# Performance work log

Measured on AMD Instinct MI355X. Metric: run time of the kernel, lower is better.

## Reference

```python
import jax, jax.numpy as jnp
import numpy as np
import math

DIM = 512
HEADS = 8
B = 16
P = 2048
REL_MAX = 64
REL_SIZE = 2 * REL_MAX + 1
RANK = 4
ALPHA = 16.0
QBITS = 4


def simq(w, bits=QBITS):
    # symmetric linear fake-quantization (matches simulate_quantization)
    qmin = -2 ** (bits - 1)
    qmax = 2 ** (bits - 1) - 1
    m = jnp.max(jnp.abs(w))
    scale = m / qmax
    q = jnp.clip(jnp.round(w / (scale + 1e-8)), qmin, qmax) * scale
    return jnp.where(m == 0, w, q)


def lora_lin(x, W, b, A, LB):
    # F.linear with quantized weight/bias + LoRA path
    out = x @ simq(W).T + simq(b)
    return out + (x @ A.T @ LB.T) * (ALPHA / RANK)


def setup_inputs() -> dict:
    key = jax.random.key(0)
    ks = jax.random.split(key, 20)
    d2 = DIM * 2
    inp = {
        "curr_pos": 2048,
        "z_curr_ri": jax.random.normal(ks[0], (B, DIM, 2), jnp.float32),
        "z_past_ri": jax.random.normal(ks[1], (P, B, DIM, 2), jnp.float32),
        "rel_bias_ri": jax.random.normal(ks[2], (REL_SIZE, DIM, 2), jnp.float32) * 0.02,
    }
    names = ["q", "k", "v", "o"]
    for i, n in enumerate(names):
        kw, ka, kb = jax.random.split(ks[3 + i], 3)
        inp["W" + n] = jax.random.normal(kw, (d2, d2), jnp.float32) / math.sqrt(d2)
        inp["b" + n] = jnp.zeros((d2,), jnp.float32)
        inp["A" + n] = jax.random.normal(ka, (RANK, d2), jnp.float32) / math.sqrt(d2)
        inp["LB" + n] = jax.random.normal(kb, (d2, RANK), jnp.float32) * 0.01
    return inp


def reference(curr_pos, z_curr_ri, z_past_ri, rel_bias_ri,
              Wq, bq, Aq, LBq, Wk, bk, Ak, LBk,
              Wv, bv, Av, LBv, Wo, bo, Ao, LBo):
    Bsz = z_curr_ri.shape[0]
    past_len = z_past_ri.shape[0]
    dim = z_curr_ri.shape[1]
    hd = dim // HEADS

    # projections on real-view of complex inputs ([.., dim, 2] -> [.., 2*dim])
    q = lora_lin(z_curr_ri.reshape(Bsz, dim * 2), Wq, bq, Aq, LBq)
    k = lora_lin(z_past_ri.reshape(past_len, Bsz, dim * 2), Wk, bk, Ak, LBk)
    v = lora_lin(z_past_ri.reshape(past_len, Bsz, dim * 2), Wv, bv, Av, LBv)

    q = q.reshape(Bsz, HEADS, hd, 2)            # [B,H,hd,2]
    k = k.reshape(past_len, Bsz, HEADS, hd, 2)  # [P,B,H,hd,2]
    v = v.reshape(past_len, Bsz, HEADS, hd, 2)
    qr, qi = q[..., 0], q[..., 1]
    kr, ki = k[..., 0], k[..., 1]
    vr, vi = v[..., 0], v[..., 1]

    # Re(q * conj(k)) summed over head_dim -> [B,H,P]
    dot = jnp.einsum('bhd,pbhd->bhp', qr, kr) + jnp.einsum('bhd,pbhd->bhp', qi, ki)

    # relative positional bias lookup (clamped index)
    rel_d = jnp.arange(curr_pos - past_len, curr_pos)
    idx = jnp.clip(rel_d + REL_MAX, 0, rel_bias_ri.shape[0] - 1)
    rb = rel_bias_ri[idx].reshape(past_len, HEADS, hd, 2)  # [P,H,hd,2]
    rel = jnp.einsum('bhd,phd->bhp', qr, rb[..., 0]) + jnp.einsum('bhd,phd->bhp', qi, rb[..., 1])

    w = jax.nn.softmax((dot + rel) / math.sqrt(hd), axis=-1)  # [B,H,P]

    # real softmax weights applied to complex values
    out_r = jnp.einsum('bhp,pbhd->bhd', w, vr)
    out_i = jnp.einsum('bhp,pbhd->bhd', w, vi)
    out_ri = jnp.stack([out_r, out_i], axis=-1).reshape(Bsz, dim * 2)

    o = lora_lin(out_ri, Wo, bo, Ao, LBo)
    return o.reshape(Bsz, dim, 2)  # real view of complex output [B,dim]
```

## Files before the change

kernel.cpp:

```cpp
#include <hip/hip_runtime.h>
#include <math.h>

typedef _Float16 f16;
typedef _Float16 f16x8 __attribute__((ext_vector_type(8)));
typedef _Float16 f16x4 __attribute__((ext_vector_type(4)));
typedef float f32x4 __attribute__((ext_vector_type(4)));

#define NP 2048
#define M_ROWS 32768

#define OFF_ABSMAX 0u
#define OFF_TQ     256u
#define OFF_TO     512u
#define OFF_QBIAS  1024u
#define OFF_XQH    32768u
#define OFF_XQL    65536u
#define OFF_XOH    98304u
#define OFF_XOL    131072u
#define OFF_QBUF   163840u
#define OFF_ATT    229376u
#define OFF_PM     294912u
#define OFF_PL     299008u
#define OFF_PO     303104u
#define OFF_WH     1048576u
#define OFF_TK     9437184u
#define OFF_TV     9961472u
#define OFF_KV     10485760u

__device__ __forceinline__ float qint_of(float w, float scale) {
    return fminf(7.f, fmaxf(-8.f, rintf(w / (scale + 1e-8f))));
}

__device__ __forceinline__ void gload16(const void* g, void* l) {
  __builtin_amdgcn_global_load_lds((const __attribute__((address_space(1))) void*)g,
                                   (__attribute__((address_space(3))) void*)l, 16, 0, 0);
}

__global__ void __launch_bounds__(256) absmax_kernel(
    const float* __restrict__ W0, const float* __restrict__ W1,
    const float* __restrict__ W2, const float* __restrict__ W3,
    unsigned* __restrict__ absmax) {
  int mat = blockIdx.x >> 6;
  int blk = blockIdx.x & 63;
  const float* W = mat == 0 ? W0 : mat == 1 ? W1 : mat == 2 ? W2 : W3;
  int tid = blk * 256 + threadIdx.x;
  const float4* W4 = (const float4*)W;
  float m = 0.f;
  #pragma unroll
  for (int i = 0; i < 16; ++i) {
    float4 v = W4[tid + i * 16384];
    m = fmaxf(m, fmaxf(fmaxf(fabsf(v.x), fabsf(v.y)), fmaxf(fabsf(v.z), fabsf(v.w))));
  }
  #pragma unroll
  for (int k = 32; k >= 1; k >>= 1) m = fmaxf(m, __shfl_xor(m, k));
  __shared__ float sm[4];
  if ((threadIdx.x & 63) == 0) sm[threadIdx.x >> 6] = m;
  __syncthreads();
  if (threadIdx.x == 0) {
    m = fmaxf(fmaxf(sm[0], sm[1]), fmaxf(sm[2], sm[3]));
    atomicMax(&absmax[mat], __float_as_uint(m));
  }
}

__global__ void __launch_bounds__(256) bias_quant_kernel(
    const float* __restrict__ b0, const float* __restrict__ b1,
    const float* __restrict__ b2, const float* __restrict__ b3,
    float* __restrict__ qbias) {
  int mat = blockIdx.x;
  const float* bb = mat == 0 ? b0 : mat == 1 ? b1 : mat == 2 ? b2 : b3;
  int t = threadIdx.x;
  float4 v = ((const float4*)bb)[t];
  float m = fmaxf(fmaxf(fabsf(v.x), fabsf(v.y)), fmaxf(fabsf(v.z), fabsf(v.w)));
  #pragma unroll
  for (int k = 32; k >= 1; k >>= 1) m = fmaxf(m, __shfl_xor(m, k));
  __shared__ float sm[4];
  if ((t & 63) == 0) sm[t >> 6] = m;
  __syncthreads();
  float M = fmaxf(fmaxf(sm[0], sm[1]), fmaxf(sm[2], sm[3]));
  float scale = M * (1.0f / 7.0f);
  float4 q;
  q.x = (M == 0.f) ? v.x : qint_of(v.x, scale) * scale;
  q.y = (M == 0.f) ? v.y : qint_of(v.y, scale) * scale;
  q.z = (M == 0.f) ? v.z : qint_of(v.z, scale) * scale;
  q.w = (M == 0.f) ? v.w : qint_of(v.w, scale) * scale;
  ((float4*)(qbias + mat * 1024))[t] = q;
}

__global__ void __launch_bounds__(256) quantW_kernel(
    const float* __restrict__ W0, const float* __restrict__ W1,
    const float* __restrict__ W2, const float* __restrict__ W3,
    const unsigned* __restrict__ absmax, f16* __restrict__ Wh) {
  int gid = blockIdx.x * 256 + threadIdx.x;
  int mat = gid >> 18;
  int idx = gid & 262143;
  const float* W = mat == 0 ? W0 : mat == 1 ? W1 : mat == 2 ? W2 : W3;
  float scale = __uint_as_float(absmax[mat]) * (1.0f / 7.0f);
  float4 v = ((const float4*)W)[idx];
  f16x4 r;
  r[0] = (f16)qint_of(v.x, scale);
  r[1] = (f16)qint_of(v.y, scale);
  r[2] = (f16)qint_of(v.z, scale);
  r[3] = (f16)qint_of(v.w, scale);
  *(f16x4*)(Wh + (size_t)mat * 1048576 + (size_t)idx * 4) = r;
}

__global__ void __launch_bounds__(256) cvt_hilo_kernel(
    const float* __restrict__ x, f16* __restrict__ hi, f16* __restrict__ lo) {
  int i = blockIdx.x * 256 + threadIdx.x;
  float4 v = ((const float4*)x)[i];
  f16 h0 = (f16)v.x, h1 = (f16)v.y, h2 = (f16)v.z, h3 = (f16)v.w;
  f16x4 hv = {h0, h1, h2, h3};
  f16x4 lv = {(f16)(v.x - (float)h0), (f16)(v.y - (float)h1),
              (f16)(v.z - (float)h2), (f16)(v.w - (float)h3)};
  *(f16x4*)(hi + (size_t)i * 4) = hv;
  *(f16x4*)(lo + (size_t)i * 4) = lv;
}

__global__ void __launch_bounds__(256) lora_t_small_kernel(
    const float* __restrict__ x, const float* __restrict__ A, float* __restrict__ t) {
  int tt = threadIdx.x;
  int b = tt >> 4;
  int r = (tt >> 2) & 3;
  int s = tt & 3;
  const float4* xv = (const float4*)(x + b * 1024 + s * 256);
  const float4* av = (const float4*)(A + r * 1024 + s * 256);
  float acc = 0.f;
  #pragma unroll 4
  for (int i = 0; i < 64; ++i) {
    float4 a = xv[i], c = av[i];
    acc += a.x * c.x + a.y * c.y + a.z * c.z + a.w * c.w;
  }
  acc += __shfl_xor(acc, 1);
  acc += __shfl_xor(acc, 2);
  if (s == 0) t[b * 4 + r] = acc;
}

__global__ void __launch_bounds__(256) lora_t_big_kernel(
    const float* __restrict__ zp, const float* __restrict__ Ak,
    const float* __restrict__ Av, float* __restrict__ tk, float* __restrict__ tv,
    f16* __restrict__ zph, f16* __restrict__ zpl) {
  __shared__ float sA[8 * 1024];
  for (int i = 0; i < 8; ++i) {
    int f4 = threadIdx.x + i * 256;
    float4 v = (f4 < 1024) ? ((const float4*)Ak)[f4] : ((const float4*)Av)[f4 - 1024];
    ((float4*)sA)[f4] = v;
  }
  __syncthreads();
  int lane = threadIdx.x & 63, wave = threadIdx.x >> 6;
  for (int it = 0; it < 4; ++it) {
    int m = blockIdx.x * 16 + wave * 4 + it;
    const float4* xr = (const float4*)(zp + (size_t)m * 1024);
    float acc[8] = {0.f, 0.f, 0.f, 0.f, 0.f, 0.f, 0.f, 0.f};
    for (int c = lane; c < 256; c += 64) {
      float4 xv = xr[c];
      if (zph) {
        f16 h0 = (f16)xv.x, h1 = (f16)xv.y, h2 = (f16)xv.z, h3 = (f16)xv.w;
        f16x4 hv = {h0, h1, h2, h3};
        f16x4 lv = {(f16)(xv.x - (float)h0), (f16)(xv.y - (float)h1),
                    (f16)(xv.z - (float)h2), (f16)(xv.w - (float)h3)};
        *(f16x4*)(zph + (size_t)m * 1024 + c * 4) = hv;
        *(f16x4*)(zpl + (size_t)m * 1024 + c * 4) = lv;
      }
      #pragma unroll
      for (int r = 0; r < 8; ++r) {
        float4 a = ((const float4*)sA)[r * 256 + c];
        acc[r] += xv.x * a.x + xv.y * a.y + xv.z * a.z + xv.w * a.w;
      }
    }
    #pragma unroll
    for (int k = 32; k >= 1; k >>= 1) {
      #pragma unroll
      for (int r = 0; r < 8; ++r) acc[r] += __shfl_xor(acc[r], k);
    }
    if (lane == 0) {
      tk[m * 4 + 0] = acc[0]; tk[m * 4 + 1] = acc[1];
      tk[m * 4 + 2] = acc[2]; tk[m * 4 + 3] = acc[3];
      tv[m * 4 + 0] = acc[4]; tv[m * 4 + 1] = acc[5];
      tv[m * 4 + 2] = acc[6]; tv[m * 4 + 3] = acc[7];
    }
  }
}

__global__ void __launch_bounds__(256) gemv_mfma_kernel(
    const f16* __restrict__ xhi, const f16* __restrict__ xlo,
    const f16* __restrict__ Wm, const unsigned* __restrict__ absmax, int mat,
    const float* __restrict__ qb, const float* __restrict__ t,
    const float* __restrict__ LB, float* __restrict__ out) {
  int wave = threadIdx.x >> 6, lane = threadIdx.x & 63;
  int nf = blockIdx.x * 4 + wave;
  int n0 = nf * 16;
  int row = lane & 15, kq = lane >> 4;
  f32x4 acc = {0.f, 0.f, 0.f, 0.f};
  const f16* xh = xhi + row * 1024 + kq * 8;
  const f16* xl = xlo + row * 1024 + kq * 8;
  const f16* wp = Wm + (size_t)(n0 + row) * 1024 + kq * 8;
  #pragma unroll 4
  for (int k0 = 0; k0 < 1024; k0 += 32) {
    f16x8 ah = *(const f16x8*)(xh + k0);
    f16x8 al = *(const f16x8*)(xl + k0);
    f16x8 bb = *(const f16x8*)(wp + k0);
    acc = __builtin_amdgcn_mfma_f32_16x16x32_f16(ah, bb, acc, 0, 0, 0);
    acc = __builtin_amdgcn_mfma_f32_16x16x32_f16(al, bb, acc, 0, 0, 0);
  }
  float scale = __uint_as_float(absmax[mat]) * (1.0f / 7.0f);
  int col = n0 + row;
  float bias = qb[col];
  float4 lb = *(const float4*)(LB + col * 4);
  #pragma unroll
  for (int j = 0; j < 4; ++j) {
    int m = kq * 4 + j;
    float4 tvv = *(const float4*)(t + m * 4);
    out[m * 1024 + col] =
        scale * acc[j] + bias + 4.0f * (tvv.x * lb.x + tvv.y * lb.y + tvv.z * lb.z + tvv.w * lb.w);
  }
}

__global__ void __launch_bounds__(256, 2) kv_gemm_kernel(
    const float* __restrict__ zp, const f16* __restrict__ Wh,
    const unsigned* __restrict__ absmax, const float* __restrict__ qbias,
    const float* __restrict__ tk, const float* __restrict__ tv,
    const float* __restrict__ LBk, const float* __restrict__ LBv,
    f16* __restrict__ kout, f16* __restrict__ vout) {
  __shared__ __align__(16) f16 sAh[128][40];
  __shared__ __align__(16) f16 sAl[128][40];
  __shared__ __align__(16) f16 sB[128][40];
  __shared__ float sT[128][4];

  int nb = blockIdx.x;
  int m0 = blockIdx.y * 128;
  bool is_v = nb >= 8;
  int n0 = (nb & 7) * 128;
  int mat = is_v ? 2 : 1;
  const f16* Wm = Wh + (size_t)mat * 1048576;
  const float* ttv = is_v ? tv : tk;
  const float* LBm = is_v ? LBv : LBk;
  const float* qb = qbias + mat * 1024;
  f16* outp = is_v ? vout : kout;

  int tid = threadIdx.x;
  int lane = tid & 63, wave = tid >> 6;
  int wm = (wave >> 1) * 64, wn = (wave & 1) * 64;
  int row = lane & 15, kq = lane >> 4;

  f32x4 acc[4][4];
  #pragma unroll
  for (int i = 0; i < 4; ++i)
    #pragma unroll
    for (int j = 0; j < 4; ++j) acc[i][j] = (f32x4){0.f, 0.f, 0.f, 0.f};

  int sr = tid >> 1, seg = tid & 1;
  const float* asrc = zp + (size_t)(m0 + sr) * 1024 + seg * 16;
  const f16* bsrc = Wm + (size_t)(n0 + sr) * 1024 + seg * 16;

  for (int k0 = 0; k0 < 1024; k0 += 32) {
    __syncthreads();
    float xs[16];
    const float4* a4 = (const float4*)(asrc + k0);
    *(float4*)&xs[0] = a4[0];
    *(float4*)&xs[4] = a4[1];
    *(float4*)&xs[8] = a4[2];
    *(float4*)&xs[12] = a4[3];
    f16 hs[16], ls[16];
    #pragma unroll
    for (int i = 0; i < 16; ++i) {
      f16 h = (f16)xs[i];
      hs[i] = h;
      ls[i] = (f16)(xs[i] - (float)h);
    }
    *(f16x8*)&sAh[sr][seg * 16] = *(f16x8*)&hs[0];
    *(f16x8*)&sAh[sr][seg * 16 + 8] = *(f16x8*)&hs[8];
    *(f16x8*)&sAl[sr][seg * 16] = *(f16x8*)&ls[0];
    *(f16x8*)&sAl[sr][seg * 16 + 8] = *(f16x8*)&ls[8];
    const f16x8* b8 = (const f16x8*)(bsrc + k0);
    *(f16x8*)&sB[sr][seg * 16] = b8[0];
    *(f16x8*)&sB[sr][seg * 16 + 8] = b8[1];
    __syncthreads();
    f16x8 ah[4], al[4], bf[4];
    #pragma unroll
    for (int mi = 0; mi < 4; ++mi) {
      ah[mi] = *(const f16x8*)&sAh[wm + mi * 16 + row][kq * 8];
      al[mi] = *(const f16x8*)&sAl[wm + mi * 16 + row][kq * 8];
    }
    #pragma unroll
    for (int ni = 0; ni < 4; ++ni) bf[ni] = *(const f16x8*)&sB[wn + ni * 16 + row][kq * 8];
    #pragma unroll
    for (int mi = 0; mi < 4; ++mi)
      #pragma unroll
      for (int ni = 0; ni < 4; ++ni)
        acc[mi][ni] = __builtin_amdgcn_mfma_f32_16x16x32_f16(ah[mi], bf[ni], acc[mi][ni], 0, 0, 0);
    #pragma unroll
    for (int mi = 0; mi < 4; ++mi)
      #pragma unroll
      for (int ni = 0; ni < 4; ++ni)
        acc[mi][ni] = __builtin_amdgcn_mfma_f32_16x16x32_f16(al[mi], bf[ni], acc[mi][ni], 0, 0, 0);
  }
  ((float2*)sT)[tid] = ((const float2*)(ttv + (size_t)m0 * 4))[tid];
  __syncthreads();
  float scale = __uint_as_float(absmax[mat]) * (1.0f / 7.0f);
  #pragma unroll
  for (int ni = 0; ni < 4; ++ni) {
    int ncol = n0 + wn + ni * 16 + row;
    int h = ncol >> 7, d = ncol & 127;
    float4 lb = *(const float4*)(LBm + ncol * 4);
    float bias = qb[ncol];
    #pragma unroll
    for (int mi = 0; mi < 4; ++mi) {
      #pragma unroll
      for (int j = 0; j < 4; ++j) {
        int mloc = wm + mi * 16 + kq * 4 + j;
        int m = m0 + mloc;
        int p = m >> 4, b = m & 15;
        float4 t4 = *(const float4*)&sT[mloc][0];
        float val = scale * acc[mi][ni][j] + bias +
                    4.0f * (t4.x * lb.x + t4.y * lb.y + t4.z * lb.z + t4.w * lb.w);
        outp[(((size_t)(b * 8 + h)) * 2048 + p) * 128 + d] = (f16)val;
      }
    }
  }
}

__global__ void __launch_bounds__(256, 3) kv_gemm_fast_kernel(
    const f16* __restrict__ zph, const f16* __restrict__ zpl,
    const f16* __restrict__ Wh, const unsigned* __restrict__ absmax,
    const float* __restrict__ qbias, const float* __restrict__ tk,
    const float* __restrict__ tv, const float* __restrict__ LBk,
    const float* __restrict__ LBv, f16* __restrict__ kout, f16* __restrict__ vout) {
  __shared__ __align__(16) f16 sbuf[24576];
  __shared__ float sT[128][4];

  int linear = blockIdx.x + (blockIdx.y << 4);
  int xcd = linear & 7;
  int slot = linear >> 3;
  int nb = slot & 15;
  int g = ((slot >> 4) << 3) + xcd;
  int m0 = g << 7;

  bool is_v = nb >= 8;
  int n0 = (nb & 7) * 128;
  int mat = is_v ? 2 : 1;
  int h = nb & 7;
  const f16* Wm = Wh + (size_t)mat * 1048576;
  const float* ttv = is_v ? tv : tk;
  const float* LBm = is_v ? LBv : LBk;
  const float* qb = qbias + mat * 1024;
  f16* outp = is_v ? vout : kout;

  int tid = threadIdx.x;
  int lane = tid & 63, wave = tid >> 6;
  int wm = (wave >> 1) * 64, wn = (wave & 1) * 64;
  int row = lane & 15, kq = lane >> 4;

  const f16* src0 = zph + (size_t)m0 * 1024;
  const f16* src1 = zpl + (size_t)m0 * 1024;
  const f16* src2 = Wm + (size_t)n0 * 1024;

  int goff[2], lbase[2];
  #pragma unroll
  for (int r = 0; r < 2; ++r) {
    int L = r * 256 + tid;
    int rw = L >> 2, cc = L & 3;
    int cs = cc ^ (rw & 3) ^ ((rw >> 2) & 3);
    goff[r] = rw * 1024 + cs * 8;
    lbase[r] = r * 2048 + wave * 512;
  }

  f32x4 acc[4][4];
  #pragma unroll
  for (int i = 0; i < 4; ++i)
    #pragma unroll
    for (int j = 0; j < 4; ++j) acc[i][j] = (f32x4){0.f, 0.f, 0.f, 0.f};

  int radA[4], radB[4];
  #pragma unroll
  for (int mi = 0; mi < 4; ++mi) {
    int R = wm + mi * 16 + row;
    radA[mi] = R * 32 + ((kq ^ (R & 3) ^ ((R >> 2) & 3)) << 3);
    int Rb = wn + mi * 16 + row;
    radB[mi] = Rb * 32 + ((kq ^ (Rb & 3) ^ ((Rb >> 2) & 3)) << 3);
  }

  #pragma unroll
  for (int r = 0; r < 2; ++r) {
    gload16(src0 + goff[r], sbuf + lbase[r]);
    gload16(src1 + goff[r], sbuf + 4096 + lbase[r]);
    gload16(src2 + goff[r], sbuf + 8192 + lbase[r]);
  }
  __syncthreads();

  int cur = 0;
  for (int t = 0; t < 32; ++t) {
    if (t < 31) {
      int nxt = (cur ^ 1) * 12288;
      int gk = (t + 1) * 32;
      #pragma unroll
      for (int r = 0; r < 2; ++r) {
        gload16(src0 + goff[r] + gk, sbuf + nxt + lbase[r]);
        gload16(src1 + goff[r] + gk, sbuf + nxt + 4096 + lbase[r]);
        gload16(src2 + goff[r] + gk, sbuf + nxt + 8192 + lbase[r]);
      }
    }
    const f16* bAh = sbuf + cur * 12288;
    const f16* bAl = bAh + 4096;
    const f16* bB = bAh + 8192;
    f16x8 ah[4], al[4], bf[4];
    #pragma unroll
    for (int mi = 0; mi < 4; ++mi) {
      ah[mi] = *(const f16x8*)&bAh[radA[mi]];
      al[mi] = *(const f16x8*)&bAl[radA[mi]];
    }
    #pragma unroll
    for (int ni = 0; ni < 4; ++ni) bf[ni] = *(const f16x8*)&bB[radB[ni]];
    #pragma unroll
    for (int mi = 0; mi < 4; ++mi)
      #pragma unroll
      for (int ni = 0; ni < 4; ++ni)
        acc[mi][ni] = __builtin_amdgcn_mfma_f32_16x16x32_f16(ah[mi], bf[ni], acc[mi][ni], 0, 0, 0);
    #pragma unroll
    for (int mi = 0; mi < 4; ++mi)
      #pragma unroll
      for (int ni = 0; ni < 4; ++ni)
        acc[mi][ni] = __builtin_amdgcn_mfma_f32_16x16x32_f16(al[mi], bf[ni], acc[mi][ni], 0, 0, 0);
    __syncthreads();
    cur ^= 1;
  }

  ((float2*)sT)[tid] = ((const float2*)(ttv + (size_t)m0 * 4))[tid];
  __syncthreads();
  float scale = __uint_as_float(absmax[mat]) * (1.0f / 7.0f);
  float biasv[4];
  float4 lbv[4];
  #pragma unroll
  for (int ni = 0; ni < 4; ++ni) {
    int ncol = n0 + wn + ni * 16 + row;
    biasv[ni] = qb[ncol];
    lbv[ni] = *(const float4*)(LBm + ncol * 4);
  }
  float* tbuf = (float*)sbuf;
  int lh = lane >> 5, l5 = lane & 31;
  #pragma unroll
  for (int halfsel = 0; halfsel < 2; ++halfsel) {
    __syncthreads();
    if ((wave >> 1) == halfsel) {
      #pragma unroll
      for (int ni = 0; ni < 4; ++ni) {
        #pragma unroll
        for (int mi = 0; mi < 4; ++mi) {
          #pragma unroll
          for (int j = 0; j < 4; ++j) {
            int ml = mi * 16 + kq * 4 + j;
            float4 t4 = *(const float4*)&sT[wm + ml][0];
            tbuf[ml * 132 + wn + ni * 16 + row] =
                scale * acc[mi][ni][j] + biasv[ni] +
                4.0f * (t4.x * lbv[ni].x + t4.y * lbv[ni].y + t4.z * lbv[ni].z +
                        t4.w * lbv[ni].w);
          }
        }
      }
    }
    __syncthreads();
    #pragma unroll
    for (int it = 0; it < 8; ++it) {
      int ml = it * 8 + wave * 2 + lh;
      int m = m0 + halfsel * 64 + ml;
      int p = m >> 4, b = m & 15;
      float4 v = *(const float4*)&tbuf[ml * 132 + l5 * 4];
      f16x4 hv = {(f16)v.x, (f16)v.y, (f16)v.z, (f16)v.w};
      *(f16x4*)(outp + (((size_t)(b * 8 + h)) * 2048 + p) * 128 + l5 * 4) = hv;
    }
  }
}

__device__ __forceinline__ float4 ld4h(const f16* p) {
  f16x4 v = *reinterpret_cast<const f16x4*>(p);
  return make_float4((float)v[0], (float)v[1], (float)v[2], (float)v[3]);
}

__global__ void __launch_bounds__(256) attn_part_kernel(
    const float* __restrict__ qbuf, const f16* __restrict__ kbuf,
    const f16* __restrict__ vbuf, const float* __restrict__ rel_bias,
    const int* __restrict__ curr_pos_p, float* __restrict__ m_part,
    float* __restrict__ l_part, float* __restrict__ o_part) {
  __shared__ float sS[256];
  __shared__ float red[8];
  __shared__ float sOv[8][132];
  int bh = blockIdx.x;
  int c = blockIdx.y;
  int b = bh >> 3, h = bh & 7;
  int p0 = c * 256;
  int tid = threadIdx.x, lane = tid & 63, wave = tid >> 6;
  int j4 = lane & 31, ph = lane >> 5;
  float4 qv = *(const float4*)(qbuf + b * 1024 + h * 128 + j4 * 4);
  int off = *curr_pos_p - NP + 64;
  const f16* kb = kbuf + ((size_t)bh * 2048 + p0) * 128;
  for (int i = 0; i < 32; ++i) {
    int pl = i * 8 + wave * 2 + ph;
    float4 kv = ld4h(kb + (size_t)pl * 128 + j4 * 4);
    int idx = min(max(p0 + pl + off, 0), 128);
    float4 rb = *(const float4*)(rel_bias + idx * 1024 + h * 128 + j4 * 4);
    float a = qv.x * (kv.x + rb.x) + qv.y * (kv.y + rb.y) +
              qv.z * (kv.z + rb.z) + qv.w * (kv.w + rb.w);
    a += __shfl_xor(a, 16);
    a += __shfl_xor(a, 8);
    a += __shfl_xor(a, 4);
    a += __shfl_xor(a, 2);
    a += __shfl_xor(a, 1);
    if (j4 == 0) sS[pl] = a * 0.125f;
  }
  __syncthreads();
  float v = sS[tid];
  float mx = v;
  #pragma unroll
  for (int k = 32; k >= 1; k >>= 1) mx = fmaxf(mx, __shfl_xor(mx, k));
  if (lane == 0) red[wave] = mx;
  __syncthreads();
  mx = fmaxf(fmaxf(red[0], red[1]), fmaxf(red[2], red[3]));
  float e = expf(v - mx);
  sS[tid] = e;
  float sum = e;
  #pragma unroll
  for (int k = 32; k >= 1; k >>= 1) sum += __shfl_xor(sum, k);
  if (lane == 0) red[4 + wave] = sum;
  __syncthreads();
  float l = red[4] + red[5] + red[6] + red[7];
  int d4 = tid & 31, pg = tid >> 5;
  const f16* vb = vbuf + ((size_t)bh * 2048 + p0 + pg * 32) * 128;
  float4 a4 = make_float4(0.f, 0.f, 0.f, 0.f);
  #pragma unroll 4
  for (int i = 0; i < 32; ++i) {
    float s = sS[pg * 32 + i];
    float4 vv = ld4h(vb + (size_t)i * 128 + d4 * 4);
    a4.x += s * vv.x;
    a4.y += s * vv.y;
    a4.z += s * vv.z;
    a4.w += s * vv.w;
  }
  *(float4*)&sOv[pg][d4 * 4] = a4;
  __syncthreads();
  if (tid < 128) {
    float o = 0.f;
    #pragma unroll
    for (int gI = 0; gI < 8; ++gI) o += sOv[gI][tid];
    int pc = bh * 8 + c;
    o_part[pc * 128 + tid] = o;
    if (tid == 0) {
      m_part[pc] = mx;
      l_part[pc] = l;
    }
  }
}

__global__ void __launch_bounds__(128) attn_combine_kernel(
    const float* __restrict__ m_part, const float* __restrict__ l_part,
    const float* __restrict__ o_part, float* __restrict__ attout) {
  int bh = blockIdx.x;
  int d = threadIdx.x;
  float M = -1e30f;
  #pragma unroll
  for (int c = 0; c < 8; ++c) M = fmaxf(M, m_part[bh * 8 + c]);
  float L = 0.f, o = 0.f;
  #pragma unroll
  for (int c = 0; c < 8; ++c) {
    float w = expf(m_part[bh * 8 + c] - M);
    L += w * l_part[bh * 8 + c];
    o += w * o_part[(bh * 8 + c) * 128 + d];
  }
  int b = bh >> 3, h = bh & 7;
  attout[b * 1024 + h * 128 + d] = o / L;
}

extern "C" void kernel_launch(void* const* d_in, const int* in_sizes, int n_in,
                              void* d_out, int out_size, void* d_ws, size_t ws_size,
                              hipStream_t stream) {
  const int* curr_pos = (const int*)d_in[0];
  const float* z_curr = (const float*)d_in[1];
  const float* z_past = (const float*)d_in[2];
  const float* rel_bias = (const float*)d_in[3];
  const float* Wq = (const float*)d_in[4];
  const float* bq = (const float*)d_in[5];
  const float* Aq = (const float*)d_in[6];
  const float* LBq = (const float*)d_in[7];
  const float* Wk = (const float*)d_in[8];
  const float* bk = (const float*)d_in[9];
  const float* Ak = (const float*)d_in[10];
  const float* LBk = (const float*)d_in[11];
  const float* Wv = (const float*)d_in[12];
  const float* bv = (const float*)d_in[13];
  const float* Av = (const float*)d_in[14];
  const float* LBv = (const float*)d_in[15];
  const float* Wo = (const float*)d_in[16];
  const float* bo = (const float*)d_in[17];
  const float* Ao = (const float*)d_in[18];
  const float* LBo = (const float*)d_in[19];

  char* ws = (char*)d_ws;
  unsigned* absmax = (unsigned*)(ws + OFF_ABSMAX);
  float* t_q = (float*)(ws + OFF_TQ);
  float* t_o = (float*)(ws + OFF_TO);
  float* qbias = (float*)(ws + OFF_QBIAS);
  f16* xqh = (f16*)(ws + OFF_XQH);
  f16* xql = (f16*)(ws + OFF_XQL);
  f16* xoh = (f16*)(ws + OFF_XOH);
  f16* xol = (f16*)(ws + OFF_XOL);
  float* qbuf = (float*)(ws + OFF_QBUF);
  float* attout = (float*)(ws + OFF_ATT);
  float* pm = (float*)(ws + OFF_PM);
  float* pl = (float*)(ws + OFF_PL);
  float* po = (float*)(ws + OFF_PO);
  f16* Wh = (f16*)(ws + OFF_WH);
  float* t_k = (float*)(ws + OFF_TK);
  float* t_v = (float*)(ws + OFF_TV);
  char* kvbase = ws + OFF_KV;

  f16* kb = (f16*)kvbase;
  f16* vb = (f16*)(kvbase + 67108864ull);
  f16* zph = (f16*)(kvbase + 2ull * 67108864ull);
  f16* zpl = (f16*)(kvbase + 3ull * 67108864ull);
  bool fast = ws_size >= (size_t)OFF_KV + 4ull * 67108864ull;

  hipMemsetAsync(absmax, 0, 16, stream);
  absmax_kernel<<<256, 256, 0, stream>>>(Wq, Wk, Wv, Wo, absmax);
  bias_quant_kernel<<<4, 256, 0, stream>>>(bq, bk, bv, bo, qbias);
  quantW_kernel<<<4096, 256, 0, stream>>>(Wq, Wk, Wv, Wo, absmax, Wh);
  cvt_hilo_kernel<<<16, 256, 0, stream>>>(z_curr, xqh, xql);
  lora_t_small_kernel<<<1, 256, 0, stream>>>(z_curr, Aq, t_q);
  gemv_mfma_kernel<<<16, 256, 0, stream>>>(xqh, xql, Wh, absmax, 0, qbias, t_q, LBq, qbuf);
  lora_t_big_kernel<<<2048, 256, 0, stream>>>(z_past, Ak, Av, t_k, t_v,
                                              fast ? zph : nullptr, fast ? zpl : nullptr);
  if (fast)
    kv_gemm_fast_kernel<<<dim3(16, 256), 256, 0, stream>>>(
        zph, zpl, Wh, absmax, qbias, t_k, t_v, LBk, LBv, kb, vb);
  else
    kv_gemm_kernel<<<dim3(16, 256), 256, 0, stream>>>(
        z_past, Wh, absmax, qbias, t_k, t_v, LBk, LBv, kb, vb);
  attn_part_kernel<<<dim3(128, 8), 256, 0, stream>>>(
      qbuf, kb, vb, rel_bias, curr_pos, pm, pl, po);
  attn_combine_kernel<<<128, 128, 0, stream>>>(pm, pl, po, attout);
  cvt_hilo_kernel<<<16, 256, 0, stream>>>(attout, xoh, xol);
  lora_t_small_kernel<<<1, 256, 0, stream>>>(attout, Ao, t_o);
  gemv_mfma_kernel<<<16, 256, 0, stream>>>(xoh, xol, Wh + 3ull * 1048576ull, absmax, 3,
                                           qbias + 3 * 1024, t_o, LBo, (float*)d_out);
}
```

Measured before the change: 823.3 us.

## Interleave hi/lo activation split along K and duplicate weights for single-MFMA stream

The K/V GEMM input is now stored as one interleaved f16 buffer (hi,lo pairs along K), and the Wk/Wv weights are written with each element duplicated, so the GEMM runs one MFMA stream over a doubled K instead of two passes that share a B fragment. The loader moves to 64-wide K tiles with an 8-way XOR swizzle, uses a larger LDS buffer, and lowers the occupancy hint from 3 to 2. Separately, the small hi/lo conversion kernels are removed and the split is done inline in the GEMV. The cost is that weight reads double and the workspace holds an extra duplicated weight copy.

Result: faster. 753.0 us (-8.5%).

```diff
diff --git a/kernel.cpp b/kernel.cpp
--- a/kernel.cpp
+++ b/kernel.cpp
@@ -13,10 +13,6 @@
 #define OFF_TQ     256u
 #define OFF_TO     512u
 #define OFF_QBIAS  1024u
-#define OFF_XQH    32768u
-#define OFF_XQL    65536u
-#define OFF_XOH    98304u
-#define OFF_XOL    131072u
 #define OFF_QBUF   163840u
 #define OFF_ATT    229376u
 #define OFF_PM     294912u
@@ -89,7 +85,8 @@
 __global__ void __launch_bounds__(256) quantW_kernel(
     const float* __restrict__ W0, const float* __restrict__ W1,
     const float* __restrict__ W2, const float* __restrict__ W3,
-    const unsigned* __restrict__ absmax, f16* __restrict__ Wh) {
+    const unsigned* __restrict__ absmax, f16* __restrict__ Wh,
+    f16* __restrict__ WD) {
   int gid = blockIdx.x * 256 + threadIdx.x;
   int mat = gid >> 18;
   int idx = gid & 262143;
@@ -102,18 +99,11 @@
   r[2] = (f16)qint_of(v.z, scale);
   r[3] = (f16)qint_of(v.w, scale);
   *(f16x4*)(Wh + (size_t)mat * 1048576 + (size_t)idx * 4) = r;
-}
-
-__global__ void __launch_bounds__(256) cvt_hilo_kernel(
-    const float* __restrict__ x, f16* __restrict__ hi, f16* __restrict__ lo) {
-  int i = blockIdx.x * 256 + threadIdx.x;
-  float4 v = ((const float4*)x)[i];
-  f16 h0 = (f16)v.x, h1 = (f16)v.y, h2 = (f16)v.z, h3 = (f16)v.w;
-  f16x4 hv = {h0, h1, h2, h3};
-  f16x4 lv = {(f16)(v.x - (float)h0), (f16)(v.y - (float)h1),
-              (f16)(v.z - (float)h2), (f16)(v.w - (float)h3)};
-  *(f16x4*)(hi + (size_t)i * 4) = hv;
-  *(f16x4*)(lo + (size_t)i * 4) = lv;
+  if (WD != nullptr && (mat == 1 || mat == 2)) {
+    f16x8 d = {r[0], r[0], r[1], r[1], r[2], r[2], r[3], r[3]};
+    int n = idx >> 8, c4 = idx & 255;
+    *(f16x8*)(WD + (size_t)(mat - 1) * 2097152 + (size_t)n * 2048 + c4 * 8) = d;
+  }
 }
 
 __global__ void __launch_bounds__(256) lora_t_small_kernel(
@@ -138,7 +128,7 @@
 __global__ void __launch_bounds__(256) lora_t_big_kernel(
     const float* __restrict__ zp, const float* __restrict__ Ak,
     const float* __restrict__ Av, float* __restrict__ tk, float* __restrict__ tv,
-    f16* __restrict__ zph, f16* __restrict__ zpl) {
+    f16* __restrict__ zpi) {
   __shared__ float sA[8 * 1024];
   for (int i = 0; i < 8; ++i) {
     int f4 = threadIdx.x + i * 256;
@@ -153,13 +143,11 @@
     float acc[8] = {0.f, 0.f, 0.f, 0.f, 0.f, 0.f, 0.f, 0.f};
     for (int c = lane; c < 256; c += 64) {
       float4 xv = xr[c];
-      if (zph) {
+      if (zpi) {
         f16 h0 = (f16)xv.x, h1 = (f16)xv.y, h2 = (f16)xv.z, h3 = (f16)xv.w;
-        f16x4 hv = {h0, h1, h2, h3};
-        f16x4 lv = {(f16)(xv.x - (float)h0), (f16)(xv.y - (float)h1),
-                    (f16)(xv.z - (float)h2), (f16)(xv.w - (float)h3)};
-        *(f16x4*)(zph + (size_t)m * 1024 + c * 4) = hv;
-        *(f16x4*)(zpl + (size_t)m * 1024 + c * 4) = lv;
+        f16x8 iv = {h0, (f16)(xv.x - (float)h0), h1, (f16)(xv.y - (float)h1),
+                    h2, (f16)(xv.z - (float)h2), h3, (f16)(xv.w - (float)h3)};
+        *(f16x8*)(zpi + (size_t)m * 2048 + c * 8) = iv;
       }
       #pragma unroll
       for (int r = 0; r < 8; ++r) {
@@ -182,8 +170,8 @@
 }
 
 __global__ void __launch_bounds__(256) gemv_mfma_kernel(
-    const f16* __restrict__ xhi, const f16* __restrict__ xlo,
-    const f16* __restrict__ Wm, const unsigned* __restrict__ absmax, int mat,
+    const float* __restrict__ x, const f16* __restrict__ Wm,
+    const unsigned* __restrict__ absmax, int mat,
     const float* __restrict__ qb, const float* __restrict__ t,
     const float* __restrict__ LB, float* __restrict__ out) {
   int wave = threadIdx.x >> 6, lane = threadIdx.x & 63;
@@ -191,13 +179,19 @@
   int n0 = nf * 16;
   int row = lane & 15, kq = lane >> 4;
   f32x4 acc = {0.f, 0.f, 0.f, 0.f};
-  const f16* xh = xhi + row * 1024 + kq * 8;
-  const f16* xl = xlo + row * 1024 + kq * 8;
+  const float* xp = x + row * 1024 + kq * 8;
   const f16* wp = Wm + (size_t)(n0 + row) * 1024 + kq * 8;
   #pragma unroll 4
   for (int k0 = 0; k0 < 1024; k0 += 32) {
-    f16x8 ah = *(const f16x8*)(xh + k0);
-    f16x8 al = *(const f16x8*)(xl + k0);
+    float4 a0 = *(const float4*)(xp + k0);
+    float4 a1 = *(const float4*)(xp + k0 + 4);
+    f16 h0 = (f16)a0.x, h1 = (f16)a0.y, h2 = (f16)a0.z, h3 = (f16)a0.w;
+    f16 h4 = (f16)a1.x, h5 = (f16)a1.y, h6 = (f16)a1.z, h7 = (f16)a1.w;
+    f16x8 ah = {h0, h1, h2, h3, h4, h5, h6, h7};
+    f16x8 al = {(f16)(a0.x - (float)h0), (f16)(a0.y - (float)h1),
+                (f16)(a0.z - (float)h2), (f16)(a0.w - (float)h3),
+                (f16)(a1.x - (float)h4), (f16)(a1.y - (float)h5),
+                (f16)(a1.z - (float)h6), (f16)(a1.w - (float)h7)};
     f16x8 bb = *(const f16x8*)(wp + k0);
     acc = __builtin_amdgcn_mfma_f32_16x16x32_f16(ah, bb, acc, 0, 0, 0);
     acc = __builtin_amdgcn_mfma_f32_16x16x32_f16(al, bb, acc, 0, 0, 0);
@@ -319,13 +313,13 @@
   }
 }
 
-__global__ void __launch_bounds__(256, 3) kv_gemm_fast_kernel(
-    const f16* __restrict__ zph, const f16* __restrict__ zpl,
-    const f16* __restrict__ Wh, const unsigned* __restrict__ absmax,
-    const float* __restrict__ qbias, const float* __restrict__ tk,
-    const float* __restrict__ tv, const float* __restrict__ LBk,
-    const float* __restrict__ LBv, f16* __restrict__ kout, f16* __restrict__ vout) {
-  __shared__ __align__(16) f16 sbuf[24576];
+__global__ void __launch_bounds__(256, 2) kv_gemm_fast_kernel(
+    const f16* __restrict__ zpi, const f16* __restrict__ WD,
+    const unsigned* __restrict__ absmax, const float* __restrict__ qbias,
+    const float* __restrict__ tk, const float* __restrict__ tv,
+    const float* __restrict__ LBk, const float* __restrict__ LBv,
+    f16* __restrict__ kout, f16* __restrict__ vout) {
+  __shared__ __align__(16) f16 sbuf[32768];
   __shared__ float sT[128][4];
 
   int linear = blockIdx.x + (blockIdx.y << 4);
@@ -339,7 +333,6 @@
   int n0 = (nb & 7) * 128;
   int mat = is_v ? 2 : 1;
   int h = nb & 7;
-  const f16* Wm = Wh + (size_t)mat * 1048576;
   const float* ttv = is_v ? tv : tk;
   const float* LBm = is_v ? LBv : LBk;
   const float* qb = qbias + mat * 1024;
@@ -350,17 +343,15 @@
   int wm = (wave >> 1) * 64, wn = (wave & 1) * 64;
   int row = lane & 15, kq = lane >> 4;
 
-  const f16* src0 = zph + (size_t)m0 * 1024;
-  const f16* src1 = zpl + (size_t)m0 * 1024;
-  const f16* src2 = Wm + (size_t)n0 * 1024;
-
-  int goff[2], lbase[2];
-  #pragma unroll
-  for (int r = 0; r < 2; ++r) {
+  const f16* srcA = zpi + (size_t)m0 * 2048;
+  const f16* srcB = WD + (size_t)(is_v ? 1 : 0) * 2097152 + (size_t)n0 * 2048;
+
+  int goff[4], lbase[4];
+  #pragma unroll
+  for (int r = 0; r < 4; ++r) {
     int L = r * 256 + tid;
-    int rw = L >> 2, cc = L & 3;
-    int cs = cc ^ (rw & 3) ^ ((rw >> 2) & 3);
-    goff[r] = rw * 1024 + cs * 8;
+    int rw = L >> 3, cc = L & 7, cs = cc ^ (rw & 7);
+    goff[r] = rw * 2048 + cs * 8;
     lbase[r] = r * 2048 + wave * 512;
   }
 
@@ -370,56 +361,52 @@
     #pragma unroll
     for (int j = 0; j < 4; ++j) acc[i][j] = (f32x4){0.f, 0.f, 0.f, 0.f};
 
-  int radA[4], radB[4];
+  int radA[8], radB[8];
   #pragma unroll
   for (int mi = 0; mi < 4; ++mi) {
-    int R = wm + mi * 16 + row;
-    radA[mi] = R * 32 + ((kq ^ (R & 3) ^ ((R >> 2) & 3)) << 3);
+    int Ra = wm + mi * 16 + row;
     int Rb = wn + mi * 16 + row;
-    radB[mi] = Rb * 32 + ((kq ^ (Rb & 3) ^ ((Rb >> 2) & 3)) << 3);
-  }
-
-  #pragma unroll
-  for (int r = 0; r < 2; ++r) {
-    gload16(src0 + goff[r], sbuf + lbase[r]);
-    gload16(src1 + goff[r], sbuf + 4096 + lbase[r]);
-    gload16(src2 + goff[r], sbuf + 8192 + lbase[r]);
+    #pragma unroll
+    for (int ks = 0; ks < 2; ++ks) {
+      radA[mi * 2 + ks] = Ra * 64 + (((ks * 4 + kq) ^ (Ra & 7)) << 3);
+      radB[mi * 2 + ks] = Rb * 64 + (((ks * 4 + kq) ^ (Rb & 7)) << 3);
+    }
+  }
+
+  #pragma unroll
+  for (int r = 0; r < 4; ++r) {
+    gload16(srcA + goff[r], sbuf + lbase[r]);
+    gload16(srcB + goff[r], sbuf + 8192 + lbase[r]);
   }
   __syncthreads();
 
   int cur = 0;
   for (int t = 0; t < 32; ++t) {
     if (t < 31) {
-      int nxt = (cur ^ 1) * 12288;
-      int gk = (t + 1) * 32;
-      #pragma unroll
-      for (int r = 0; r < 2; ++r) {
-        gload16(src0 + goff[r] + gk, sbuf + nxt + lbase[r]);
-        gload16(src1 + goff[r] + gk, sbuf + nxt + 4096 + lbase[r]);
-        gload16(src2 + goff[r] + gk, sbuf + nxt + 8192 + lbase[r]);
+      int nxt = (cur ^ 1) * 16384;
+      int gk = (t + 1) * 64;
+      #pragma unroll
+      for (int r = 0; r < 4; ++r) {
+        gload16(srcA + goff[r] + gk, sbuf + nxt + lbase[r]);
+        gload16(srcB + goff[r] + gk, sbuf + nxt + 8192 + lbase[r]);
       }
     }
-    const f16* bAh = sbuf + cur * 12288;
-    const f16* bAl = bAh + 4096;
-    const f16* bB = bAh + 8192;
-    f16x8 ah[4], al[4], bf[4];
-    #pragma unroll
-    for (int mi = 0; mi < 4; ++mi) {
-      ah[mi] = *(const f16x8*)&bAh[radA[mi]];
-      al[mi] = *(const f16x8*)&bAl[radA[mi]];
-    }
-    #pragma unroll
-    for (int ni = 0; ni < 4; ++ni) bf[ni] = *(const f16x8*)&bB[radB[ni]];
-    #pragma unroll
-    for (int mi = 0; mi < 4; ++mi)
-      #pragma unroll
-      for (int ni = 0; ni < 4; ++ni)
-        acc[mi][ni] = __builtin_amdgcn_mfma_f32_16x16x32_f16(ah[mi], bf[ni], acc[mi][ni], 0, 0, 0);
-    #pragma unroll
-    for (int mi = 0; mi < 4; ++mi)
-      #pragma unroll
-      for (int ni = 0; ni < 4; ++ni)
-        acc[mi][ni] = __builtin_amdgcn_mfma_f32_16x16x32_f16(al[mi], bf[ni], acc[mi][ni], 0, 0, 0);
+    const f16* bA = sbuf + cur * 16384;
+    const f16* bB = bA + 8192;
+    f16x8 af[8], bf[8];
+    #pragma unroll
+    for (int i = 0; i < 8; ++i) {
+      af[i] = *(const f16x8*)&bA[radA[i]];
+      bf[i] = *(const f16x8*)&bB[radB[i]];
+    }
+    #pragma unroll
+    for (int ks = 0; ks < 2; ++ks)
+      #pragma unroll
+      for (int mi = 0; mi < 4; ++mi)
+        #pragma unroll
+        for (int ni = 0; ni < 4; ++ni)
+          acc[mi][ni] = __builtin_amdgcn_mfma_f32_16x16x32_f16(
+              af[mi * 2 + ks], bf[ni * 2 + ks], acc[mi][ni], 0, 0, 0);
     __syncthreads();
     cur ^= 1;
   }
@@ -597,10 +584,6 @@
   float* t_q = (float*)(ws + OFF_TQ);
   float* t_o = (float*)(ws + OFF_TO);
   float* qbias = (float*)(ws + OFF_QBIAS);
-  f16* xqh = (f16*)(ws + OFF_XQH);
-  f16* xql = (f16*)(ws + OFF_XQL);
-  f16* xoh = (f16*)(ws + OFF_XOH);
-  f16* xol = (f16*)(ws + OFF_XOL);
   float* qbuf = (float*)(ws + OFF_QBUF);
   float* attout = (float*)(ws + OFF_ATT);
   float* pm = (float*)(ws + OFF_PM);
@@ -613,30 +596,29 @@
 
   f16* kb = (f16*)kvbase;
   f16* vb = (f16*)(kvbase + 67108864ull);
-  f16* zph = (f16*)(kvbase + 2ull * 67108864ull);
-  f16* zpl = (f16*)(kvbase + 3ull * 67108864ull);
-  bool fast = ws_size >= (size_t)OFF_KV + 4ull * 67108864ull;
+  f16* zpi = (f16*)(kvbase + 134217728ull);
+  f16* WD = (f16*)(kvbase + 268435456ull);
+  bool fast = ws_size >= (size_t)OFF_KV + 276824064ull;
 
   hipMemsetAsync(absmax, 0, 16, stream);
   absmax_kernel<<<256, 256, 0, stream>>>(Wq, Wk, Wv, Wo, absmax);
   bias_quant_kernel<<<4, 256, 0, stream>>>(bq, bk, bv, bo, qbias);
-  quantW_kernel<<<4096, 256, 0, stream>>>(Wq, Wk, Wv, Wo, absmax, Wh);
-  cvt_hilo_kernel<<<16, 256, 0, stream>>>(z_curr, xqh, xql);
+  quantW_kernel<<<4096, 256, 0, stream>>>(Wq, Wk, Wv, Wo, absmax, Wh,
+                                          fast ? WD : nullptr);
   lora_t_small_kernel<<<1, 256, 0, stream>>>(z_curr, Aq, t_q);
-  gemv_mfma_kernel<<<16, 256, 0, stream>>>(xqh, xql, Wh, absmax, 0, qbias, t_q, LBq, qbuf);
+  gemv_mfma_kernel<<<16, 256, 0, stream>>>(z_curr, Wh, absmax, 0, qbias, t_q, LBq, qbuf);
   lora_t_big_kernel<<<2048, 256, 0, stream>>>(z_past, Ak, Av, t_k, t_v,
-                                              fast ? zph : nullptr, fast ? zpl : nullptr);
+                                              fast ? zpi : nullptr);
   if (fast)
     kv_gemm_fast_kernel<<<dim3(16, 256), 256, 0, stream>>>(
-        zph, zpl, Wh, absmax, qbias, t_k, t_v, LBk, LBv, kb, vb);
+        zpi, WD, absmax, qbias, t_k, t_v, LBk, LBv, kb, vb);
   else
     kv_gemm_kernel<<<dim3(16, 256), 256, 0, stream>>>(
         z_past, Wh, absmax, qbias, t_k, t_v, LBk, LBv, kb, vb);
   attn_part_kernel<<<dim3(128, 8), 256, 0, stream>>>(
       qbuf, kb, vb, rel_bias, curr_pos, pm, pl, po);
   attn_combine_kernel<<<128, 128, 0, stream>>>(pm, pl, po, attout);
-  cvt_hilo_kernel<<<16, 256, 0, stream>>>(attout, xoh, xol);
   lora_t_small_kernel<<<1, 256, 0, stream>>>(attout, Ao, t_o);
-  gemv_mfma_kernel<<<16, 256, 0, stream>>>(xoh, xol, Wh + 3ull * 1048576ull, absmax, 3,
+  gemv_mfma_kernel<<<16, 256, 0, stream>>>(attout, Wh + 3ull * 1048576ull, absmax, 3,
                                            qbias + 3 * 1024, t_o, LBo, (float*)d_out);
 }
```
